# Kernel tuning notes

Measured on AMD Instinct MI355X. Metric: run time of the kernel, lower is better.

The kernel has to match this reference:

```python
import jax, jax.numpy as jnp
import numpy as np

NUM_HEADS = 12
SIZE_PER_HEAD = 64


def setup_inputs() -> dict:
    key = jax.random.key(0)
    ks = jax.random.split(key, 4)
    B, S, D = 4, 2048, NUM_HEADS * SIZE_PER_HEAD
    std = 0.02
    return {
        "x": jax.random.normal(ks[0], (B, S, D), dtype=jnp.float32),
        "Wq": jax.random.normal(ks[1], (D, D), dtype=jnp.float32) * std,
        "bq": jnp.zeros((D,), dtype=jnp.float32),
        "Wk": jax.random.normal(ks[2], (D, D), dtype=jnp.float32) * std,
        "bk": jnp.zeros((D,), dtype=jnp.float32),
        "Wv": jax.random.normal(ks[3], (D, D), dtype=jnp.float32) * std,
        "bv": jnp.zeros((D,), dtype=jnp.float32),
        "mask": jnp.ones((B, S), dtype=jnp.int32),
    }


def reference(x, Wq, bq, Wk, bk, Wv, bv, mask):
    B, S, Dm = x.shape
    H, Dh = NUM_HEADS, SIZE_PER_HEAD
    # QKV projections (no activation, per defaults)
    q = (x @ Wq + bq).reshape(B, S, H, Dh)
    k = (x @ Wk + bk).reshape(B, S, H, Dh)
    v = (x @ Wv + bv).reshape(B, S, H, Dh)
    # scaled dot-product scores [B, H, F, T]
    scores = jnp.einsum("bfhd,bthd->bhft", q, k) / jnp.sqrt(
        jnp.asarray(Dh, dtype=x.dtype)
    )
    # additive mask: (1 - mask) * -10000, broadcast over heads and F
    adder = (1.0 - mask.astype(x.dtype))[:, None, None, :] * -10000.0
    probs = jax.nn.softmax(scores + adder, axis=-1)
    # dropout is identity at inference (training=None)
    ctx = jnp.einsum("bhft,bthd->bfhd", probs, v)
    return ctx.reshape(B, S, H * Dh)
```

## Files before the change

### kernel.cpp

```cpp
#include <hip/hip_runtime.h>
#include <cstdint>
#include <cstddef>

#define B_  4
#define S_  2048
#define H_  12
#define DH  64
#define DM  768

typedef unsigned short u16;
typedef __bf16 bf16x8 __attribute__((ext_vector_type(8)));
typedef float f32x4 __attribute__((ext_vector_type(4)));

__device__ __forceinline__ u16 f2bf(float f) {
  unsigned u = __float_as_uint(f);
  u += 0x7FFFu + ((u >> 16) & 1u);
  return (u16)(u >> 16);
}

__device__ __forceinline__ void gl16(const u16* g, u16* l) {
  __builtin_amdgcn_global_load_lds((const __attribute__((address_space(1))) void*)g,
                                   (__attribute__((address_space(3))) void*)l,
                                   16, 0, 0);
}

__global__ __launch_bounds__(256) void k_cvt_x(const float* __restrict__ x, u16* __restrict__ xb,
                                               const int* __restrict__ mask, int* __restrict__ mflags) {
  int i = blockIdx.x * 256 + threadIdx.x;
  const float4 v = ((const float4*)x)[i];
  ushort4 o;
  o.x = f2bf(v.x); o.y = f2bf(v.y); o.z = f2bf(v.z); o.w = f2bf(v.w);
  ((ushort4*)xb)[i] = o;
  if (blockIdx.x < 64) {
    __shared__ int f;
    if (threadIdx.x == 0) f = 0;
    __syncthreads();
    if (threadIdx.x < 128 && mask[blockIdx.x * 128 + threadIdx.x] != 1) f = 1;
    __syncthreads();
    if (threadIdx.x == 0) mflags[blockIdx.x] = f;
  }
}

__global__ __launch_bounds__(256) void k_wtrans(const float* __restrict__ Wq, const float* __restrict__ Wk,
                                                const float* __restrict__ Wv, u16* __restrict__ Wt) {
  const float* W = blockIdx.z == 0 ? Wq : (blockIdx.z == 1 ? Wk : Wv);
  u16* o = Wt + (size_t)blockIdx.z * DM * DM;
  __shared__ float t[32][33];
  const int x = threadIdx.x, y = threadIdx.y;
  const int n0 = blockIdx.x * 32, k0 = blockIdx.y * 32;
#pragma unroll
  for (int i = 0; i < 4; i++)
    t[y + i*8][x] = W[(size_t)(k0 + y + i*8)*DM + n0 + x];
  __syncthreads();
#pragma unroll
  for (int i = 0; i < 4; i++)
    o[(size_t)(n0 + y + i*8)*DM + k0 + x] = f2bf(t[x][y + i*8]);
}

__global__ __launch_bounds__(256) void k_qkv(const u16* __restrict__ Xb, const u16* __restrict__ Wt,
                                             const float* __restrict__ bq, const float* __restrict__ bk,
                                             const float* __restrict__ bv, u16* __restrict__ QKV) {
  const int mat = blockIdx.z;
  const float* bias = mat == 0 ? bq : (mat == 1 ? bk : bv);
  const u16* Wm = Wt + (size_t)mat * DM * DM;
  const int n0 = blockIdx.x * 128, m0 = blockIdx.y * 128;
  __shared__ __align__(16) u16 Al[128*32];
  __shared__ __align__(16) u16 Bl[128*32];
  const int tid = threadIdx.x, w = tid >> 6, l = tid & 63, l15 = l & 15, quad = l >> 4;
  const int wm = w & 1, wn = w >> 1;
  f32x4 acc[4][4];
#pragma unroll
  for (int i = 0; i < 4; i++)
#pragma unroll
    for (int j = 0; j < 4; j++) acc[i][j] = f32x4{0.f, 0.f, 0.f, 0.f};

  for (int kt = 0; kt < DM/32; ++kt) {
    __syncthreads();
#pragma unroll
    for (int rep = 0; rep < 2; ++rep) {
      int c = tid + rep*256;
      int row = c >> 2, s = c & 3;
      int sl = s ^ ((row ^ (row >> 2)) & 3);
      gl16(Xb + (size_t)(m0 + row)*DM + kt*32 + sl*8, Al + c*8);
      gl16(Wm + (size_t)(n0 + row)*DM + kt*32 + sl*8, Bl + c*8);
    }
    __syncthreads();
    bf16x8 af[4], bfr[4];
#pragma unroll
    for (int mt = 0; mt < 4; mt++) {
      int row = wm*64 + mt*16 + l15;
      int ph = quad ^ ((row ^ (row >> 2)) & 3);
      af[mt] = *(const bf16x8*)(Al + row*32 + ph*8);
    }
#pragma unroll
    for (int nt = 0; nt < 4; nt++) {
      int row = wn*64 + nt*16 + l15;
      int ph = quad ^ ((row ^ (row >> 2)) & 3);
      bfr[nt] = *(const bf16x8*)(Bl + row*32 + ph*8);
    }
#pragma unroll
    for (int mt = 0; mt < 4; mt++)
#pragma unroll
      for (int nt = 0; nt < 4; nt++)
        acc[mt][nt] = __builtin_amdgcn_mfma_f32_16x16x32_bf16(af[mt], bfr[nt], acc[mt][nt], 0, 0, 0);
  }

  const float osc = (mat == 0) ? (0.125f * 1.44269504f) : 1.0f;
  float b4[4];
#pragma unroll
  for (int nt = 0; nt < 4; nt++) b4[nt] = bias[n0 + wn*64 + nt*16 + l15];
  u16* outm = QKV + (size_t)mat * (size_t)(B_*S_) * DM;
#pragma unroll
  for (int mt = 0; mt < 4; mt++)
#pragma unroll
    for (int r = 0; r < 4; r++) {
      int gm = m0 + wm*64 + mt*16 + quad*4 + r;
      u16* orow = outm + (size_t)gm*DM + n0 + wn*64;
#pragma unroll
      for (int nt = 0; nt < 4; nt++)
        orow[nt*16 + l15] = f2bf((acc[mt][nt][r] + b4[nt]) * osc);
    }
}

__global__ __launch_bounds__(256) void k_vtrans(const u16* __restrict__ Vb, u16* __restrict__ Vt) {
  const int bh = blockIdx.y, b = bh / H_, h = bh % H_;
  const int t0 = blockIdx.x * 64;
  __shared__ u16 tl[64][72];
  const int tid = threadIdx.x;
#pragma unroll
  for (int i = 0; i < 4; i++) {
    int idx = tid + i*256;
    int r = idx >> 4, c4 = idx & 15;
    *(ushort4*)(&tl[r][c4*4]) = *(const ushort4*)(Vb + (size_t)(b*S_ + t0 + r)*DM + h*DH + c4*4);
  }
  __syncthreads();
#pragma unroll
  for (int i = 0; i < 4; i++) {
    int idx = tid + i*256;
    int d = idx >> 4;
    int tq = (idx & 15) * 4;
    ushort4 o;
    o.x = tl[tq][d]; o.y = tl[tq+1][d]; o.z = tl[tq+2][d]; o.w = tl[tq+3][d];
    *(ushort4*)(Vt + (size_t)(bh*DH + d)*S_ + t0 + tq) = o;
  }
}

__global__ __launch_bounds__(256, 3) void k_attn(const u16* __restrict__ Qb, const u16* __restrict__ Kb,
                                                 const u16* __restrict__ Vt, const int* __restrict__ mask,
                                                 const int* __restrict__ mflags, float* __restrict__ out) {
  const int bh = blockIdx.x, b = bh / H_, h = bh % H_;
  const int q0 = blockIdx.y * 128;
  __shared__ __align__(16) u16 Kl[128*64];
  __shared__ __align__(16) u16 Vl[64*128];
  __shared__ __align__(16) u16 QP[4*32*72];
  __shared__ __align__(16) float maskl[128];
  const int tid = threadIdx.x, w = tid >> 6, l = tid & 63, l15 = l & 15, quad = l >> 4;

#pragma unroll
  for (int i = 0; i < 4; i++) {
    int c = tid + i*256;
    int r = c >> 3, s = c & 7, sl = s ^ (r & 7);
    gl16(Qb + (size_t)(b*S_ + q0 + r)*DM + h*DH + sl*8, QP + c*8);
  }
  __syncthreads();
  bf16x8 qf[2][2];
#pragma unroll
  for (int nt = 0; nt < 2; nt++)
#pragma unroll
    for (int ks = 0; ks < 2; ks++) {
      int r = w*32 + nt*16 + l15;
      int ph = (ks*4 + quad) ^ (r & 7);
      qf[nt][ks] = *(const bf16x8*)(QP + r*64 + ph*8);
    }
  __syncthreads();

  f32x4 O[2][4], Ol[2];
#pragma unroll
  for (int i = 0; i < 2; i++) {
    Ol[i] = f32x4{0.f, 0.f, 0.f, 0.f};
#pragma unroll
    for (int j = 0; j < 4; j++) O[i][j] = f32x4{0.f, 0.f, 0.f, 0.f};
  }
  bf16x8 vone;
#pragma unroll
  for (int j = 0; j < 8; j++) vone[j] = (l15 == 0) ? (__bf16)1.0f : (__bf16)0.0f;
  u16* Pw = QP + w*32*72;

  for (int tt = 0; tt < S_/128; ++tt) {
    const int t0 = tt * 128;
    __syncthreads();
#pragma unroll
    for (int i = 0; i < 4; i++) {
      int c = tid + i*256;
      { int r = c >> 3, s = c & 7, sl = s ^ (r & 7);
        gl16(Kb + (size_t)(b*S_ + t0 + r)*DM + h*DH + sl*8, Kl + c*8); }
      { int r = c >> 4, s = c & 15, sl = s ^ (r & 15);
        gl16(Vt + (size_t)(bh*DH + r)*S_ + t0 + sl*8, Vl + c*8); }
    }
    const int mflag = mflags[b*16 + tt];
    if (mflag) {
      if (tid < 128)
        maskl[tid] = (1.0f - (float)mask[b*S_ + t0 + tid]) * (-10000.0f * 1.44269504f);
    }
    __syncthreads();

#pragma unroll
    for (int h2 = 0; h2 < 2; ++h2) {
      f32x4 sc[4][2];
#pragma unroll
      for (int i = 0; i < 4; i++) { sc[i][0] = f32x4{0.f,0.f,0.f,0.f}; sc[i][1] = f32x4{0.f,0.f,0.f,0.f}; }
#pragma unroll
      for (int mt = 0; mt < 4; mt++) {
        int row = h2*64 + mt*16 + l15;
        bf16x8 k0f = *(const bf16x8*)(Kl + row*64 + ((quad    ) ^ (row & 7))*8);
        bf16x8 k1f = *(const bf16x8*)(Kl + row*64 + ((4 + quad) ^ (row & 7))*8);
#pragma unroll
        for (int nt = 0; nt < 2; nt++) {
          sc[mt][nt] = __builtin_amdgcn_mfma_f32_16x16x32_bf16(k0f, qf[nt][0], sc[mt][nt], 0, 0, 0);
          sc[mt][nt] = __builtin_amdgcn_mfma_f32_16x16x32_bf16(k1f, qf[nt][1], sc[mt][nt], 0, 0, 0);
        }
      }
      if (mflag) {
#pragma unroll
        for (int mt = 0; mt < 4; mt++) {
          f32x4 mv = *(const f32x4*)&maskl[h2*64 + mt*16 + quad*4];
#pragma unroll
          for (int nt = 0; nt < 2; nt++)
#pragma unroll
            for (int r = 0; r < 4; r++) sc[mt][nt][r] += mv[r];
        }
      }
#pragma unroll
      for (int nt = 0; nt < 2; nt++)
#pragma unroll
        for (int mt = 0; mt < 4; mt++) {
          unsigned u[4];
#pragma unroll
          for (int r = 0; r < 4; r++) u[r] = __float_as_uint(exp2f(sc[mt][nt][r]));
          uint2 pk;
          pk.x = __builtin_amdgcn_perm(u[1], u[0], 0x07060302u);
          pk.y = __builtin_amdgcn_perm(u[3], u[2], 0x07060302u);
          *(uint2*)(Pw + (nt*16 + l15)*72 + mt*16 + quad*4) = pk;
        }
      asm volatile("s_waitcnt lgkmcnt(0)" ::: "memory");
#pragma unroll
      for (int kk = 0; kk < 2; kk++) {
        int ksg = h2*2 + kk;
        bf16x8 pa[2], vb[4];
#pragma unroll
        for (int mo = 0; mo < 2; mo++)
          pa[mo] = *(const bf16x8*)(Pw + (mo*16 + l15)*72 + kk*32 + quad*8);
#pragma unroll
        for (int nd = 0; nd < 4; nd++) {
          int d = nd*16 + l15;
          int ph = (ksg*4 + quad) ^ (d & 15);
          vb[nd] = *(const bf16x8*)(Vl + d*128 + ph*8);
        }
#pragma unroll
        for (int mo = 0; mo < 2; mo++) {
#pragma unroll
          for (int nd = 0; nd < 4; nd++)
            O[mo][nd] = __builtin_amdgcn_mfma_f32_16x16x32_bf16(pa[mo], vb[nd], O[mo][nd], 0, 0, 0);
          Ol[mo] = __builtin_amdgcn_mfma_f32_16x16x32_bf16(pa[mo], vone, Ol[mo], 0, 0, 0);
        }
      }
    }
  }

#pragma unroll
  for (int mo = 0; mo < 2; mo++)
#pragma unroll
    for (int r = 0; r < 4; r++) {
      float lsum = __shfl(Ol[mo][r], l & 48);
      float inv = 1.0f / lsum;
      int q = q0 + w*32 + mo*16 + quad*4 + r;
      float* orow = out + (size_t)(b*S_ + q)*DM + h*DH;
#pragma unroll
      for (int nd = 0; nd < 4; nd++)
        orow[nd*16 + l15] = O[mo][nd][r] * inv;
    }
}

extern "C" void kernel_launch(void* const* d_in, const int* in_sizes, int n_in,
                              void* d_out, int out_size, void* d_ws, size_t ws_size,
                              hipStream_t stream) {
  const float* x  = (const float*)d_in[0];
  const float* Wq = (const float*)d_in[1];
  const float* bq = (const float*)d_in[2];
  const float* Wk = (const float*)d_in[3];
  const float* bk = (const float*)d_in[4];
  const float* Wv = (const float*)d_in[5];
  const float* bv = (const float*)d_in[6];
  const int* mask = (const int*)d_in[7];
  float* out = (float*)d_out;

  u16* Xb  = (u16*)d_ws;
  u16* Wt  = Xb  + (size_t)B_*S_*DM;
  u16* QKV = Wt  + (size_t)3*DM*DM;
  u16* Vt  = QKV + (size_t)3*B_*S_*DM;
  int* mflags = (int*)(Vt + (size_t)B_*S_*DM);

  k_cvt_x <<<dim3((B_*S_*DM)/1024), dim3(256), 0, stream>>>(x, Xb, mask, mflags);
  k_wtrans<<<dim3(24, 24, 3), dim3(32, 8), 0, stream>>>(Wq, Wk, Wv, Wt);
  k_qkv   <<<dim3(6, 64, 3), dim3(256), 0, stream>>>(Xb, Wt, bq, bk, bv, QKV);
  k_vtrans<<<dim3(S_/64, B_*H_), dim3(256), 0, stream>>>(QKV + (size_t)2*B_*S_*DM, Vt);
  k_attn  <<<dim3(B_*H_, S_/128), dim3(256), 0, stream>>>(QKV, QKV + (size_t)B_*S_*DM, Vt, mask, mflags, out);
}
```

Measured before the change: 224.6 us.

## Fuse V transpose into QKV GEMM epilogue and widen K tile to 64

The QKV GEMM now writes the V projection directly in transposed [b,h,d,t] layout, which removes the separate k_vtrans kernel and its extra read and write of V. The GEMM K-step goes from 32 to 64 with an 8-way XOR swizzle, halving the number of barrier pairs. Global load offsets are precomputed and pointers advanced incrementally in both GEMM and attention. The first score MFMA now takes a zero constant instead of a zero-initialised accumulator. Shared memory per GEMM block doubles, and the transposed V stores are 8-byte scattered writes.

```diff
diff --git a/kernel.cpp b/kernel.cpp
--- a/kernel.cpp
+++ b/kernel.cpp
@@ -59,13 +59,13 @@
 
 __global__ __launch_bounds__(256) void k_qkv(const u16* __restrict__ Xb, const u16* __restrict__ Wt,
                                              const float* __restrict__ bq, const float* __restrict__ bk,
-                                             const float* __restrict__ bv, u16* __restrict__ QKV) {
+                                             const float* __restrict__ bv, u16* __restrict__ QKV,
+                                             u16* __restrict__ Vt) {
   const int mat = blockIdx.z;
   const float* bias = mat == 0 ? bq : (mat == 1 ? bk : bv);
-  const u16* Wm = Wt + (size_t)mat * DM * DM;
   const int n0 = blockIdx.x * 128, m0 = blockIdx.y * 128;
-  __shared__ __align__(16) u16 Al[128*32];
-  __shared__ __align__(16) u16 Bl[128*32];
+  __shared__ __align__(16) u16 Al[128*64];
+  __shared__ __align__(16) u16 Bl[128*64];
   const int tid = threadIdx.x, w = tid >> 6, l = tid & 63, l15 = l & 15, quad = l >> 4;
   const int wm = w & 1, wn = w >> 1;
   f32x4 acc[4][4];
@@ -74,74 +74,83 @@
 #pragma unroll
     for (int j = 0; j < 4; j++) acc[i][j] = f32x4{0.f, 0.f, 0.f, 0.f};
 
-  for (int kt = 0; kt < DM/32; ++kt) {
-    __syncthreads();
-#pragma unroll
-    for (int rep = 0; rep < 2; ++rep) {
-      int c = tid + rep*256;
-      int row = c >> 2, s = c & 3;
-      int sl = s ^ ((row ^ (row >> 2)) & 3);
-      gl16(Xb + (size_t)(m0 + row)*DM + kt*32 + sl*8, Al + c*8);
-      gl16(Wm + (size_t)(n0 + row)*DM + kt*32 + sl*8, Bl + c*8);
-    }
-    __syncthreads();
-    bf16x8 af[4], bfr[4];
-#pragma unroll
-    for (int mt = 0; mt < 4; mt++) {
-      int row = wm*64 + mt*16 + l15;
-      int ph = quad ^ ((row ^ (row >> 2)) & 3);
-      af[mt] = *(const bf16x8*)(Al + row*32 + ph*8);
-    }
-#pragma unroll
-    for (int nt = 0; nt < 4; nt++) {
-      int row = wn*64 + nt*16 + l15;
-      int ph = quad ^ ((row ^ (row >> 2)) & 3);
-      bfr[nt] = *(const bf16x8*)(Bl + row*32 + ph*8);
-    }
+  int loff[4];
+#pragma unroll
+  for (int i = 0; i < 4; i++) {
+    int c = tid + i*256;
+    int r = c >> 3, s = c & 7, sl = s ^ (r & 7);
+    loff[i] = r*DM + sl*8;
+  }
+  const u16* ap = Xb + (size_t)m0 * DM;
+  const u16* bp = Wt + (size_t)mat * DM * DM + (size_t)n0 * DM;
+
+  for (int kt = 0; kt < DM/64; ++kt) {
+    __syncthreads();
+#pragma unroll
+    for (int i = 0; i < 4; i++) {
+      int c = tid + i*256;
+      gl16(ap + loff[i], Al + c*8);
+      gl16(bp + loff[i], Bl + c*8);
+    }
+    ap += 64; bp += 64;
+    __syncthreads();
+#pragma unroll
+    for (int ks = 0; ks < 2; ++ks) {
+      bf16x8 af[4], bfr[4];
+#pragma unroll
+      for (int mt = 0; mt < 4; mt++) {
+        int row = wm*64 + mt*16 + l15;
+        int ph = (ks*4 + quad) ^ (row & 7);
+        af[mt] = *(const bf16x8*)(Al + row*64 + ph*8);
+      }
+#pragma unroll
+      for (int nt = 0; nt < 4; nt++) {
+        int row = wn*64 + nt*16 + l15;
+        int ph = (ks*4 + quad) ^ (row & 7);
+        bfr[nt] = *(const bf16x8*)(Bl + row*64 + ph*8);
+      }
+#pragma unroll
+      for (int mt = 0; mt < 4; mt++)
+#pragma unroll
+        for (int nt = 0; nt < 4; nt++)
+          acc[mt][nt] = __builtin_amdgcn_mfma_f32_16x16x32_bf16(af[mt], bfr[nt], acc[mt][nt], 0, 0, 0);
+    }
+  }
+
+  float b4[4];
+#pragma unroll
+  for (int nt = 0; nt < 4; nt++) b4[nt] = bias[n0 + wn*64 + nt*16 + l15];
+
+  if (mat == 2) {
+    const int b = m0 / S_;
+    const int h = (n0 + wn*64) >> 6;
+    const int tbase = (m0 % S_) + wm*64;
 #pragma unroll
     for (int mt = 0; mt < 4; mt++)
 #pragma unroll
-      for (int nt = 0; nt < 4; nt++)
-        acc[mt][nt] = __builtin_amdgcn_mfma_f32_16x16x32_bf16(af[mt], bfr[nt], acc[mt][nt], 0, 0, 0);
-  }
-
-  const float osc = (mat == 0) ? (0.125f * 1.44269504f) : 1.0f;
-  float b4[4];
-#pragma unroll
-  for (int nt = 0; nt < 4; nt++) b4[nt] = bias[n0 + wn*64 + nt*16 + l15];
-  u16* outm = QKV + (size_t)mat * (size_t)(B_*S_) * DM;
-#pragma unroll
-  for (int mt = 0; mt < 4; mt++)
-#pragma unroll
-    for (int r = 0; r < 4; r++) {
-      int gm = m0 + wm*64 + mt*16 + quad*4 + r;
-      u16* orow = outm + (size_t)gm*DM + n0 + wn*64;
-#pragma unroll
-      for (int nt = 0; nt < 4; nt++)
-        orow[nt*16 + l15] = f2bf((acc[mt][nt][r] + b4[nt]) * osc);
-    }
-}
-
-__global__ __launch_bounds__(256) void k_vtrans(const u16* __restrict__ Vb, u16* __restrict__ Vt) {
-  const int bh = blockIdx.y, b = bh / H_, h = bh % H_;
-  const int t0 = blockIdx.x * 64;
-  __shared__ u16 tl[64][72];
-  const int tid = threadIdx.x;
-#pragma unroll
-  for (int i = 0; i < 4; i++) {
-    int idx = tid + i*256;
-    int r = idx >> 4, c4 = idx & 15;
-    *(ushort4*)(&tl[r][c4*4]) = *(const ushort4*)(Vb + (size_t)(b*S_ + t0 + r)*DM + h*DH + c4*4);
-  }
-  __syncthreads();
-#pragma unroll
-  for (int i = 0; i < 4; i++) {
-    int idx = tid + i*256;
-    int d = idx >> 4;
-    int tq = (idx & 15) * 4;
-    ushort4 o;
-    o.x = tl[tq][d]; o.y = tl[tq+1][d]; o.z = tl[tq+2][d]; o.w = tl[tq+3][d];
-    *(ushort4*)(Vt + (size_t)(bh*DH + d)*S_ + t0 + tq) = o;
+      for (int nt = 0; nt < 4; nt++) {
+        int d = nt*16 + l15;
+        int t = tbase + mt*16 + quad*4;
+        ushort4 o;
+        o.x = f2bf(acc[mt][nt][0] + b4[nt]);
+        o.y = f2bf(acc[mt][nt][1] + b4[nt]);
+        o.z = f2bf(acc[mt][nt][2] + b4[nt]);
+        o.w = f2bf(acc[mt][nt][3] + b4[nt]);
+        *(ushort4*)(Vt + ((size_t)(b*H_ + h)*DH + d)*S_ + t) = o;
+      }
+  } else {
+    const float osc = (mat == 0) ? (0.125f * 1.44269504f) : 1.0f;
+    u16* outm = QKV + (size_t)mat * (size_t)(B_*S_) * DM;
+#pragma unroll
+    for (int mt = 0; mt < 4; mt++)
+#pragma unroll
+      for (int r = 0; r < 4; r++) {
+        int gm = m0 + wm*64 + mt*16 + quad*4 + r;
+        u16* orow = outm + (size_t)gm*DM + n0 + wn*64;
+#pragma unroll
+        for (int nt = 0; nt < 4; nt++)
+          orow[nt*16 + l15] = f2bf((acc[mt][nt][r] + b4[nt]) * osc);
+      }
   }
 }
 
@@ -181,34 +190,41 @@
 #pragma unroll
     for (int j = 0; j < 4; j++) O[i][j] = f32x4{0.f, 0.f, 0.f, 0.f};
   }
+  const f32x4 ZV = {0.f, 0.f, 0.f, 0.f};
   bf16x8 vone;
 #pragma unroll
   for (int j = 0; j < 8; j++) vone[j] = (l15 == 0) ? (__bf16)1.0f : (__bf16)0.0f;
   u16* Pw = QP + w*32*72;
 
+  int koff[4], voff[4];
+#pragma unroll
+  for (int i = 0; i < 4; i++) {
+    int c = tid + i*256;
+    { int r = c >> 3, s = c & 7, sl = s ^ (r & 7);   koff[i] = r*DM + sl*8; }
+    { int r = c >> 4, s = c & 15, sl = s ^ (r & 15); voff[i] = r*S_ + sl*8; }
+  }
+  const u16* kp = Kb + (size_t)(b*S_)*DM + h*DH;
+  const u16* vp = Vt + (size_t)bh*DH*S_;
+
   for (int tt = 0; tt < S_/128; ++tt) {
-    const int t0 = tt * 128;
     __syncthreads();
 #pragma unroll
     for (int i = 0; i < 4; i++) {
       int c = tid + i*256;
-      { int r = c >> 3, s = c & 7, sl = s ^ (r & 7);
-        gl16(Kb + (size_t)(b*S_ + t0 + r)*DM + h*DH + sl*8, Kl + c*8); }
-      { int r = c >> 4, s = c & 15, sl = s ^ (r & 15);
-        gl16(Vt + (size_t)(bh*DH + r)*S_ + t0 + sl*8, Vl + c*8); }
-    }
+      gl16(kp + koff[i], Kl + c*8);
+      gl16(vp + voff[i], Vl + c*8);
+    }
+    kp += 128*DM; vp += 128;
     const int mflag = mflags[b*16 + tt];
     if (mflag) {
       if (tid < 128)
-        maskl[tid] = (1.0f - (float)mask[b*S_ + t0 + tid]) * (-10000.0f * 1.44269504f);
+        maskl[tid] = (1.0f - (float)mask[b*S_ + tt*128 + tid]) * (-10000.0f * 1.44269504f);
     }
     __syncthreads();
 
 #pragma unroll
     for (int h2 = 0; h2 < 2; ++h2) {
       f32x4 sc[4][2];
-#pragma unroll
-      for (int i = 0; i < 4; i++) { sc[i][0] = f32x4{0.f,0.f,0.f,0.f}; sc[i][1] = f32x4{0.f,0.f,0.f,0.f}; }
 #pragma unroll
       for (int mt = 0; mt < 4; mt++) {
         int row = h2*64 + mt*16 + l15;
@@ -216,7 +232,7 @@
         bf16x8 k1f = *(const bf16x8*)(Kl + row*64 + ((4 + quad) ^ (row & 7))*8);
 #pragma unroll
         for (int nt = 0; nt < 2; nt++) {
-          sc[mt][nt] = __builtin_amdgcn_mfma_f32_16x16x32_bf16(k0f, qf[nt][0], sc[mt][nt], 0, 0, 0);
+          sc[mt][nt] = __builtin_amdgcn_mfma_f32_16x16x32_bf16(k0f, qf[nt][0], ZV, 0, 0, 0);
           sc[mt][nt] = __builtin_amdgcn_mfma_f32_16x16x32_bf16(k1f, qf[nt][1], sc[mt][nt], 0, 0, 0);
         }
       }
@@ -302,7 +318,6 @@
 
   k_cvt_x <<<dim3((B_*S_*DM)/1024), dim3(256), 0, stream>>>(x, Xb, mask, mflags);
   k_wtrans<<<dim3(24, 24, 3), dim3(32, 8), 0, stream>>>(Wq, Wk, Wv, Wt);
-  k_qkv   <<<dim3(6, 64, 3), dim3(256), 0, stream>>>(Xb, Wt, bq, bk, bv, QKV);
-  k_vtrans<<<dim3(S_/64, B_*H_), dim3(256), 0, stream>>>(QKV + (size_t)2*B_*S_*DM, Vt);
+  k_qkv   <<<dim3(6, 64, 3), dim3(256), 0, stream>>>(Xb, Wt, bq, bk, bv, QKV, Vt);
   k_attn  <<<dim3(B_*H_, S_/128), dim3(256), 0, stream>>>(QKV, QKV + (size_t)B_*S_*DM, Vt, mask, mflags, out);
 }
```

After: 216.5 us. 3.6% less time.
